# Performance work log

Measured on AMD Instinct MI355X. Metric: run time of the kernel, lower is better.

## Reference

```python
import jax, jax.numpy as jnp
import numpy as np

B, L, F, H, U = 512, 64, 2048, 512, 512


def setup_inputs() -> dict:
    key = jax.random.key(0)
    ks = jax.random.split(key, 10)
    s = 0.05
    return {
        'features': jax.random.normal(ks[0], (B, L, F), jnp.float32),
        'hidden': jax.random.normal(ks[1], (B, H), jnp.float32),
        'W1': jax.random.normal(ks[2], (F, U), jnp.float32) * s,
        'b1': jnp.zeros((U,), jnp.float32),
        'W2': jax.random.normal(ks[3], (H, U), jnp.float32) * s,
        'b2': jnp.zeros((U,), jnp.float32),
        'V': jax.random.normal(ks[4], (U, 1), jnp.float32) * s,
        'bV': jnp.zeros((1,), jnp.float32),
        'W3': jax.random.normal(ks[5], (F + H, U), jnp.float32) * s,
        'b3': jnp.zeros((U,), jnp.float32),
        'ka1': jax.random.normal(ks[6], (H, L), jnp.float32) * s,
        'kb1': jax.random.normal(ks[7], (L, L), jnp.float32) * s,
        'ka2': jax.random.normal(ks[8], (H, L), jnp.float32) * s,
        'kb2': jax.random.normal(ks[9], (L, L), jnp.float32) * s,
    }


def reference(features, hidden, W1, b1, W2, b2, V, bV, W3, b3, ka1, kb1, ka2, kb2):
    # features: [B, L, F], hidden: [B, H]
    Lp = features.shape[1]
    h = hidden[:, None, :]  # [B, 1, H] = hidden_with_time_axis

    # score_model == 'default'
    score = jnp.tanh(features @ W1 + b1 + (h @ W2 + b2))  # [B, L, U]
    logits = score @ V + bV  # [B, L, 1]
    attention_weights = jax.nn.softmax(logits, axis=1)  # [B, L, 1]

    # local_att == 'True': Gaussian window re-weighting (vectorized version of
    # the original nested Python loops over (batch, position)).
    def local_p(ka, kb):
        t = jnp.tanh(h @ ka) @ kb  # [B, 1, L]
        t = jax.nn.sigmoid(t) * jnp.sqrt(jnp.float32(Lp))
        return jnp.transpose(t, (0, 2, 1))  # [B, L, 1]

    p1 = local_p(ka1, kb1)  # predicted row center, [B, L, 1]
    p2 = local_p(ka2, kb2)  # predicted col center, [B, L, 1]

    i = jnp.arange(Lp, dtype=jnp.float32)
    g = jnp.sqrt(jnp.float32(Lp))
    rows = jnp.floor((i + 1.0) / g)                 # s_t[..., 0]
    cols = jnp.floor(jnp.mod(i + 1.0, g)) - 1.0     # s_t[..., 1]
    d2 = (rows[None, :, None] - p1) ** 2 + (cols[None, :, None] - p2) ** 2  # [B, L, 1]

    D = 1.0
    attention_weights = attention_weights * jnp.exp(-d2 / (0.5 * D * D))

    context_vector = jnp.sum(attention_weights * features, axis=1)  # [B, F]

    # context_vector_concat == 'True'
    out = jnp.tanh(jnp.concatenate([context_vector, hidden], axis=-1)) @ W3 + b3  # [B, U]
    return out, attention_weights
```

## Files before the change

### kernel.cpp

```cpp
#include <hip/hip_runtime.h>

typedef __bf16 bf16x8 __attribute__((ext_vector_type(8)));
typedef float f32x4 __attribute__((ext_vector_type(4)));

static __device__ __forceinline__ unsigned short f2bf(float f) {
  union { float fv; unsigned u; } v; v.fv = f;
  unsigned u = v.u;
  u += 0x7fffu + ((u >> 16) & 1u);
  return (unsigned short)(u >> 16);
}

__global__ __launch_bounds__(256) void pack_w(const float* __restrict__ W,
                                              unsigned short* __restrict__ P) {
  __shared__ float tile[32][65];
  const int N = 512;
  int k0 = blockIdx.x * 32, n0 = blockIdx.y * 64;
  int t = threadIdx.x;
  int nn = t & 63, kkb = t >> 6;
#pragma unroll
  for (int i = 0; i < 8; ++i) {
    int kk = kkb + i * 4;
    tile[kk][nn] = W[(size_t)(k0 + kk) * N + n0 + nn];
  }
  __syncthreads();
  size_t base = (size_t)blockIdx.x * (N * 32) + (size_t)n0 * 32;
#pragma unroll
  for (int i = 0; i < 8; ++i) {
    int e = t + i * 256;
    P[base + e] = f2bf(tile[e & 31][e >> 5]);
  }
}

__global__ __launch_bounds__(128) void prep_batch(
    const float* __restrict__ hidden,
    const float* __restrict__ ka1, const float* __restrict__ kb1,
    const float* __restrict__ ka2, const float* __restrict__ kb2,
    float* __restrict__ gauss,
    unsigned short* __restrict__ hid_bf,
    unsigned short* __restrict__ A2) {
  int b = blockIdx.x, t = threadIdx.x;
  __shared__ float hl[512];
  __shared__ float tt[128];
  __shared__ float pp[128];
  for (int i = t; i < 512; i += 128) {
    float v = hidden[b * 512 + i];
    hl[i] = v;
    hid_bf[b * 512 + i] = f2bf(v);
    A2[(size_t)b * 2560 + 2048 + i] = f2bf(tanhf(v));
  }
  __syncthreads();
  {
    const float* ka = (t < 64) ? ka1 : ka2;
    int lp = t & 63;
    float s = 0.f;
    for (int h = 0; h < 512; ++h) s += hl[h] * ka[h * 64 + lp];
    tt[t] = tanhf(s);
  }
  __syncthreads();
  {
    const float* kb = (t < 64) ? kb1 : kb2;
    const float* ts = (t < 64) ? tt : tt + 64;
    int l = t & 63;
    float s = 0.f;
    for (int j = 0; j < 64; ++j) s += ts[j] * kb[j * 64 + l];
    pp[t] = 8.0f / (1.0f + expf(-s));
  }
  __syncthreads();
  if (t < 64) {
    float fi = (float)(t + 1);
    float r = floorf(fi * 0.125f);
    float c = floorf(fmodf(fi, 8.0f)) - 1.0f;
    float dr = r - pp[t], dc = c - pp[64 + t];
    gauss[b * 64 + t] = expf(-2.0f * (dr * dr + dc * dc));
  }
}

__global__ __launch_bounds__(256) void gemm64(
    const unsigned short* __restrict__ A, int K,
    const unsigned short* __restrict__ Wp,
    const float* __restrict__ bias,
    float* __restrict__ C) {
  __shared__ unsigned short lA[64 * 40];
  __shared__ unsigned short lB[64 * 40];
  int m0 = blockIdx.x * 64, n0 = blockIdx.y * 64;
  int t = threadIdx.x;
  int w = t >> 6, lane = t & 63, q = lane >> 4, l15 = lane & 15;
  f32x4 acc[4] = {};
  int arow = t >> 2, achk = (t & 3) * 8;
  int nsteps = K >> 5;
  for (int ks = 0; ks < nsteps; ++ks) {
    int k0 = ks << 5;
    int4 av = *(const int4*)(A + (size_t)(m0 + arow) * K + k0 + achk);
    int4 bvv = *(const int4*)(Wp + (size_t)ks * (512 * 32) + (size_t)n0 * 32 + t * 8);
    __syncthreads();
    *(int4*)(lA + arow * 40 + achk) = av;
    *(int4*)(lB + arow * 40 + achk) = bvv;
    __syncthreads();
    bf16x8 bf = *(const bf16x8*)(lB + (w * 16 + l15) * 40 + q * 8);
#pragma unroll
    for (int mt = 0; mt < 4; ++mt) {
      bf16x8 af = *(const bf16x8*)(lA + (mt * 16 + l15) * 40 + q * 8);
      acc[mt] = __builtin_amdgcn_mfma_f32_16x16x32_bf16(af, bf, acc[mt], 0, 0, 0);
    }
  }
  float bsv = bias[n0 + w * 16 + l15];
#pragma unroll
  for (int mt = 0; mt < 4; ++mt)
#pragma unroll
    for (int j = 0; j < 4; ++j)
      C[(size_t)(m0 + mt * 16 + q * 4 + j) * 512 + n0 + w * 16 + l15] = acc[mt][j] + bsv;
}

__global__ __launch_bounds__(512, 2) void attn_main(
    const float* __restrict__ feat,
    const unsigned short* __restrict__ W1p,
    const float* __restrict__ b1,
    const float* __restrict__ hb,
    const float* __restrict__ V,
    const float* __restrict__ bVp,
    const float* __restrict__ gauss,
    float* __restrict__ aw_out,
    unsigned short* __restrict__ A2) {
  __shared__ unsigned short lA[64 * 40];
  __shared__ unsigned short lB[512 * 40];
  __shared__ float red[64 * 8];
  __shared__ float awl[64];
  int b = blockIdx.x, t = threadIdx.x;
  int w = t >> 6, lane = t & 63, q = lane >> 4, l15 = lane & 15;
  f32x4 acc[4][4] = {};
  int arow = t >> 3, achk = t & 7;
  const float* Ab = feat + (size_t)b * (64 * 2048);
  for (int ks = 0; ks < 64; ++ks) {
    int k0 = ks << 5;
    float4 av = *(const float4*)(Ab + (size_t)arow * 2048 + k0 + achk * 4);
    const unsigned short* bp = W1p + (size_t)ks * (512 * 32);
    int4 bv0 = *(const int4*)(bp + (size_t)t * 8);
    int4 bv1 = *(const int4*)(bp + (size_t)(t + 512) * 8);
    int4 bv2 = *(const int4*)(bp + (size_t)(t + 1024) * 8);
    int4 bv3 = *(const int4*)(bp + (size_t)(t + 1536) * 8);
    __syncthreads();
    ushort4 a4;
    a4.x = f2bf(av.x); a4.y = f2bf(av.y); a4.z = f2bf(av.z); a4.w = f2bf(av.w);
    *(ushort4*)(lA + arow * 40 + achk * 4) = a4;
    {
      int c = t;
      *(int4*)(lB + (c >> 2) * 40 + (c & 3) * 8) = bv0;
      c = t + 512;
      *(int4*)(lB + (c >> 2) * 40 + (c & 3) * 8) = bv1;
      c = t + 1024;
      *(int4*)(lB + (c >> 2) * 40 + (c & 3) * 8) = bv2;
      c = t + 1536;
      *(int4*)(lB + (c >> 2) * 40 + (c & 3) * 8) = bv3;
    }
    __syncthreads();
    bf16x8 bf[4];
#pragma unroll
    for (int nt = 0; nt < 4; ++nt)
      bf[nt] = *(const bf16x8*)(lB + (w * 64 + nt * 16 + l15) * 40 + q * 8);
#pragma unroll
    for (int mt = 0; mt < 4; ++mt) {
      bf16x8 af = *(const bf16x8*)(lA + (mt * 16 + l15) * 40 + q * 8);
#pragma unroll
      for (int nt = 0; nt < 4; ++nt)
        acc[mt][nt] = __builtin_amdgcn_mfma_f32_16x16x32_bf16(af, bf[nt], acc[mt][nt], 0, 0, 0);
    }
  }
  float vv[4], bb[4];
#pragma unroll
  for (int nt = 0; nt < 4; ++nt) {
    int u = w * 64 + nt * 16 + l15;
    vv[nt] = V[u];
    bb[nt] = b1[u] + hb[b * 512 + u];
  }
#pragma unroll
  for (int mt = 0; mt < 4; ++mt) {
#pragma unroll
    for (int j = 0; j < 4; ++j) {
      float p = 0.f;
#pragma unroll
      for (int nt = 0; nt < 4; ++nt)
        p += tanhf(acc[mt][nt][j] + bb[nt]) * vv[nt];
      p += __shfl_xor(p, 1);
      p += __shfl_xor(p, 2);
      p += __shfl_xor(p, 4);
      p += __shfl_xor(p, 8);
      if (l15 == 0) red[(mt * 16 + q * 4 + j) * 8 + w] = p;
    }
  }
  __syncthreads();
  if (t < 64) {
    float s = bVp[0];
#pragma unroll
    for (int ww = 0; ww < 8; ++ww) s += red[t * 8 + ww];
    float mx = s;
#pragma unroll
    for (int o = 1; o < 64; o <<= 1) mx = fmaxf(mx, __shfl_xor(mx, o));
    float e = expf(s - mx);
    float sm = e;
#pragma unroll
    for (int o = 1; o < 64; o <<= 1) sm += __shfl_xor(sm, o);
    float a = (e / sm) * gauss[b * 64 + t];
    awl[t] = a;
    aw_out[b * 64 + t] = a;
  }
  __syncthreads();
  float4 cacc = make_float4(0.f, 0.f, 0.f, 0.f);
  for (int l = 0; l < 64; ++l) {
    float a = awl[l];
    float4 fv = *(const float4*)(Ab + (size_t)l * 2048 + t * 4);
    cacc.x += a * fv.x; cacc.y += a * fv.y; cacc.z += a * fv.z; cacc.w += a * fv.w;
  }
  ushort4 o4;
  o4.x = f2bf(tanhf(cacc.x)); o4.y = f2bf(tanhf(cacc.y));
  o4.z = f2bf(tanhf(cacc.z)); o4.w = f2bf(tanhf(cacc.w));
  *(ushort4*)(A2 + (size_t)b * 2560 + t * 4) = o4;
}

extern "C" void kernel_launch(void* const* d_in, const int* in_sizes, int n_in,
                              void* d_out, int out_size, void* d_ws, size_t ws_size,
                              hipStream_t stream) {
  (void)in_sizes; (void)n_in; (void)out_size; (void)ws_size;
  const float* feat   = (const float*)d_in[0];
  const float* hidden = (const float*)d_in[1];
  const float* W1  = (const float*)d_in[2];
  const float* b1  = (const float*)d_in[3];
  const float* W2  = (const float*)d_in[4];
  const float* b2  = (const float*)d_in[5];
  const float* V   = (const float*)d_in[6];
  const float* bV  = (const float*)d_in[7];
  const float* W3  = (const float*)d_in[8];
  const float* b3  = (const float*)d_in[9];
  const float* ka1 = (const float*)d_in[10];
  const float* kb1 = (const float*)d_in[11];
  const float* ka2 = (const float*)d_in[12];
  const float* kb2 = (const float*)d_in[13];

  char* ws = (char*)d_ws;
  unsigned short* W1p   = (unsigned short*)(ws);
  unsigned short* W2p   = (unsigned short*)(ws + 2097152);
  unsigned short* W3p   = (unsigned short*)(ws + 2621440);
  unsigned short* hidbf = (unsigned short*)(ws + 5242880);
  float*          hb    = (float*)(ws + 5767168);
  float*          gauss = (float*)(ws + 6815744);
  unsigned short* A2    = (unsigned short*)(ws + 6946816);

  float* out    = (float*)d_out;
  float* aw_out = out + 512 * 512;

  pack_w<<<dim3(64, 8), 256, 0, stream>>>(W1, W1p);
  pack_w<<<dim3(16, 8), 256, 0, stream>>>(W2, W2p);
  pack_w<<<dim3(80, 8), 256, 0, stream>>>(W3, W3p);
  prep_batch<<<512, 128, 0, stream>>>(hidden, ka1, kb1, ka2, kb2, gauss, hidbf, A2);
  gemm64<<<dim3(8, 8), 256, 0, stream>>>(hidbf, 512, W2p, b2, hb);
  attn_main<<<512, 512, 0, stream>>>(feat, W1p, b1, hb, V, bV, gauss, aw_out, A2);
  gemm64<<<dim3(8, 8), 256, 0, stream>>>(A2, 2560, W3p, b3, out);
}
```

Measured before the change: 555.7 us.

## Prefetch next K-slice in GEMM loops, merge weight packing, raise occupancy bounds

The main attention kernel and the small GEMMs now issue the global loads for the next K-step right after the LDS barrier, so they overlap with the current MFMA work (register double-buffering). Epilogue constants (V, biases, gauss, bV) are loaded before the main loop. The three weight-pack launches become one launch, and the prep dot product is split into four accumulators. Launch bounds for attn_main go from 2 to 4 waves per SIMD, which caps registers per thread and may cause spills given the 64-float accumulator plus the prefetch registers.

```diff
diff --git a/kernel.cpp b/kernel.cpp
--- a/kernel.cpp
+++ b/kernel.cpp
@@ -10,10 +10,18 @@
   return (unsigned short)(u >> 16);
 }
 
-__global__ __launch_bounds__(256) void pack_w(const float* __restrict__ W,
-                                              unsigned short* __restrict__ P) {
+__global__ __launch_bounds__(256) void pack_all(
+    const float* __restrict__ W1, const float* __restrict__ W2,
+    const float* __restrict__ W3,
+    unsigned short* __restrict__ W1p, unsigned short* __restrict__ W2p,
+    unsigned short* __restrict__ W3p) {
   __shared__ float tile[32][65];
   const int N = 512;
+  const float* W; unsigned short* P; int nk;
+  if (blockIdx.z == 0)      { W = W1; P = W1p; nk = 64; }
+  else if (blockIdx.z == 1) { W = W2; P = W2p; nk = 16; }
+  else                      { W = W3; P = W3p; nk = 80; }
+  if ((int)blockIdx.x >= nk) return;
   int k0 = blockIdx.x * 32, n0 = blockIdx.y * 64;
   int t = threadIdx.x;
   int nn = t & 63, kkb = t >> 6;
@@ -52,9 +60,14 @@
   {
     const float* ka = (t < 64) ? ka1 : ka2;
     int lp = t & 63;
-    float s = 0.f;
-    for (int h = 0; h < 512; ++h) s += hl[h] * ka[h * 64 + lp];
-    tt[t] = tanhf(s);
+    float s0 = 0.f, s1 = 0.f, s2 = 0.f, s3 = 0.f;
+    for (int h = 0; h < 512; h += 4) {
+      s0 += hl[h + 0] * ka[(h + 0) * 64 + lp];
+      s1 += hl[h + 1] * ka[(h + 1) * 64 + lp];
+      s2 += hl[h + 2] * ka[(h + 2) * 64 + lp];
+      s3 += hl[h + 3] * ka[(h + 3) * 64 + lp];
+    }
+    tt[t] = tanhf((s0 + s1) + (s2 + s3));
   }
   __syncthreads();
   {
@@ -75,7 +88,7 @@
   }
 }
 
-__global__ __launch_bounds__(256) void gemm64(
+__global__ __launch_bounds__(256, 4) void gemm64(
     const unsigned short* __restrict__ A, int K,
     const unsigned short* __restrict__ Wp,
     const float* __restrict__ bias,
@@ -88,14 +101,19 @@
   f32x4 acc[4] = {};
   int arow = t >> 2, achk = (t & 3) * 8;
   int nsteps = K >> 5;
+  const unsigned short* pA = A + (size_t)(m0 + arow) * K + achk;
+  const unsigned short* pB = Wp + (size_t)n0 * 32 + t * 8;
+  float bsv = bias[n0 + w * 16 + l15];
+  int4 av = *(const int4*)(pA);
+  int4 bvv = *(const int4*)(pB);
   for (int ks = 0; ks < nsteps; ++ks) {
-    int k0 = ks << 5;
-    int4 av = *(const int4*)(A + (size_t)(m0 + arow) * K + k0 + achk);
-    int4 bvv = *(const int4*)(Wp + (size_t)ks * (512 * 32) + (size_t)n0 * 32 + t * 8);
     __syncthreads();
     *(int4*)(lA + arow * 40 + achk) = av;
     *(int4*)(lB + arow * 40 + achk) = bvv;
     __syncthreads();
+    int ksn = (ks + 1 < nsteps) ? ks + 1 : ks;
+    av = *(const int4*)(pA + ksn * 32);
+    bvv = *(const int4*)(pB + (size_t)ksn * (512 * 32));
     bf16x8 bf = *(const bf16x8*)(lB + (w * 16 + l15) * 40 + q * 8);
 #pragma unroll
     for (int mt = 0; mt < 4; ++mt) {
@@ -103,7 +121,6 @@
       acc[mt] = __builtin_amdgcn_mfma_f32_16x16x32_bf16(af, bf, acc[mt], 0, 0, 0);
     }
   }
-  float bsv = bias[n0 + w * 16 + l15];
 #pragma unroll
   for (int mt = 0; mt < 4; ++mt)
 #pragma unroll
@@ -111,7 +128,7 @@
       C[(size_t)(m0 + mt * 16 + q * 4 + j) * 512 + n0 + w * 16 + l15] = acc[mt][j] + bsv;
 }
 
-__global__ __launch_bounds__(512, 2) void attn_main(
+__global__ __launch_bounds__(512, 4) void attn_main(
     const float* __restrict__ feat,
     const unsigned short* __restrict__ W1p,
     const float* __restrict__ b1,
@@ -130,14 +147,26 @@
   f32x4 acc[4][4] = {};
   int arow = t >> 3, achk = t & 7;
   const float* Ab = feat + (size_t)b * (64 * 2048);
+  const float* pA = Ab + (size_t)arow * 2048 + achk * 4;
+  const unsigned short* pB = W1p + (size_t)t * 8;
+
+  float vv[4], bb[4];
+#pragma unroll
+  for (int nt = 0; nt < 4; ++nt) {
+    int u = w * 64 + nt * 16 + l15;
+    vv[nt] = V[u];
+    bb[nt] = b1[u] + hb[b * 512 + u];
+  }
+  float gs = (t < 64) ? gauss[b * 64 + t] : 0.f;
+  float bV0 = bVp[0];
+
+  float4 av = *(const float4*)(pA);
+  int4 bv0 = *(const int4*)(pB);
+  int4 bv1 = *(const int4*)(pB + 4096);
+  int4 bv2 = *(const int4*)(pB + 8192);
+  int4 bv3 = *(const int4*)(pB + 12288);
+
   for (int ks = 0; ks < 64; ++ks) {
-    int k0 = ks << 5;
-    float4 av = *(const float4*)(Ab + (size_t)arow * 2048 + k0 + achk * 4);
-    const unsigned short* bp = W1p + (size_t)ks * (512 * 32);
-    int4 bv0 = *(const int4*)(bp + (size_t)t * 8);
-    int4 bv1 = *(const int4*)(bp + (size_t)(t + 512) * 8);
-    int4 bv2 = *(const int4*)(bp + (size_t)(t + 1024) * 8);
-    int4 bv3 = *(const int4*)(bp + (size_t)(t + 1536) * 8);
     __syncthreads();
     ushort4 a4;
     a4.x = f2bf(av.x); a4.y = f2bf(av.y); a4.z = f2bf(av.z); a4.w = f2bf(av.w);
@@ -153,6 +182,15 @@
       *(int4*)(lB + (c >> 2) * 40 + (c & 3) * 8) = bv3;
     }
     __syncthreads();
+    {
+      int ksn = (ks < 63) ? ks + 1 : ks;
+      const unsigned short* bp = pB + (size_t)ksn * (512 * 32);
+      av  = *(const float4*)(pA + ksn * 32);
+      bv0 = *(const int4*)(bp);
+      bv1 = *(const int4*)(bp + 4096);
+      bv2 = *(const int4*)(bp + 8192);
+      bv3 = *(const int4*)(bp + 12288);
+    }
     bf16x8 bf[4];
 #pragma unroll
     for (int nt = 0; nt < 4; ++nt)
@@ -164,13 +202,6 @@
       for (int nt = 0; nt < 4; ++nt)
         acc[mt][nt] = __builtin_amdgcn_mfma_f32_16x16x32_bf16(af, bf[nt], acc[mt][nt], 0, 0, 0);
     }
-  }
-  float vv[4], bb[4];
-#pragma unroll
-  for (int nt = 0; nt < 4; ++nt) {
-    int u = w * 64 + nt * 16 + l15;
-    vv[nt] = V[u];
-    bb[nt] = b1[u] + hb[b * 512 + u];
   }
 #pragma unroll
   for (int mt = 0; mt < 4; ++mt) {
@@ -189,7 +220,7 @@
   }
   __syncthreads();
   if (t < 64) {
-    float s = bVp[0];
+    float s = bV0;
 #pragma unroll
     for (int ww = 0; ww < 8; ++ww) s += red[t * 8 + ww];
     float mx = s;
@@ -199,7 +230,7 @@
     float sm = e;
 #pragma unroll
     for (int o = 1; o < 64; o <<= 1) sm += __shfl_xor(sm, o);
-    float a = (e / sm) * gauss[b * 64 + t];
+    float a = (e / sm) * gs;
     awl[t] = a;
     aw_out[b * 64 + t] = a;
   }
@@ -247,9 +278,7 @@
   float* out    = (float*)d_out;
   float* aw_out = out + 512 * 512;
 
-  pack_w<<<dim3(64, 8), 256, 0, stream>>>(W1, W1p);
-  pack_w<<<dim3(16, 8), 256, 0, stream>>>(W2, W2p);
-  pack_w<<<dim3(80, 8), 256, 0, stream>>>(W3, W3p);
+  pack_all<<<dim3(80, 8, 3), 256, 0, stream>>>(W1, W2, W3, W1p, W2p, W3p);
   prep_batch<<<512, 128, 0, stream>>>(hidden, ka1, kb1, ka2, kb2, gauss, hidbf, A2);
   gemm64<<<dim3(8, 8), 256, 0, stream>>>(hidbf, 512, W2p, b2, hb);
   attn_main<<<512, 512, 0, stream>>>(feat, W1p, b1, hb, V, bV, gauss, aw_out, A2);
```

Measured after the change: 542.9 us. -2.3%, faster.
